# Optimization experiments

Hardware: AMD Instinct MI355X
Metric: run time of the kernel (lower is better)

The kernel has to match this reference:

```python
import jax, jax.numpy as jnp
import numpy as np

NUM_EXPERTS = 8
TOP_K = 2
HIDDEN = 1024
INTER = 2048
SHARED_INTER = 1024
T = 8192
STD = 0.02


def setup_inputs() -> dict:
    key = jax.random.key(0)
    ks = jax.random.split(key, 6)
    return {
        "hidden_states": jax.random.normal(ks[0], (T, HIDDEN), dtype=jnp.float32),
        "w_gate": jax.random.normal(ks[1], (NUM_EXPERTS, HIDDEN), dtype=jnp.float32) * STD,
        "w_fc": jax.random.normal(ks[2], (NUM_EXPERTS, INTER, HIDDEN), dtype=jnp.float32) * STD,
        "w_proj": jax.random.normal(ks[3], (NUM_EXPERTS, HIDDEN, INTER), dtype=jnp.float32) * (STD / np.sqrt(2 * 24)),
        "w_fc_shared": jax.random.normal(ks[4], (SHARED_INTER, HIDDEN), dtype=jnp.float32) * STD,
        "w_proj_shared": jax.random.normal(ks[5], (HIDDEN, SHARED_INTER), dtype=jnp.float32) * (STD / np.sqrt(2 * 24)),
    }


def reference(hidden_states, w_gate, w_fc, w_proj, w_fc_shared, w_proj_shared):
    x = hidden_states.reshape(-1, HIDDEN)  # [T, d]
    # --- routing: top-k over router logits, softmax over the k selected logits (fp32) ---
    router_logits = x @ w_gate.T  # [T, E]
    top_vals, top_idx = jax.lax.top_k(router_logits, TOP_K)  # [T, K]
    gates = jax.nn.softmax(top_vals.astype(jnp.float32), axis=-1).astype(x.dtype)  # [T, K]
    # --- expert FFN: dense per-expert compute, masked combine (== scatter/grouped-GEMM math) ---
    out = jnp.zeros_like(x)
    for e in range(NUM_EXPERTS):
        gate_e = jnp.sum(jnp.where(top_idx == e, gates, jnp.zeros_like(gates)), axis=-1)  # [T]
        h = jax.nn.gelu(x @ w_fc[e].T, approximate=False) @ w_proj[e].T  # [T, d]
        out = out + gate_e[:, None] * h
    # --- shared expert ---
    shared = jax.nn.gelu(x @ w_fc_shared.T, approximate=False) @ w_proj_shared.T
    return out + shared
```

## Files before the change

kernel.cpp:

```cpp
#include <hip/hip_runtime.h>
#include <cstdint>
#include <cstdio>

#define DEVI __device__ __forceinline__

constexpr int TOKS = 8192;
constexpr int HID  = 1024;
constexpr int INTR = 2048;
constexpr int SINT = 1024;
constexpr int NEXP = 8;
constexpr int MAXSLOT = 17408;

typedef __bf16 bf16x8 __attribute__((ext_vector_type(8)));
typedef float  f32x4  __attribute__((ext_vector_type(4)));

DEVI unsigned short f2bf(float f) {
  unsigned int u = __float_as_uint(f);
  u += 0x7FFFu + ((u >> 16) & 1u);
  return (unsigned short)(u >> 16);
}

DEVI float bf2f(unsigned short h) {
  return __uint_as_float((unsigned int)h << 16);
}

DEVI void gl_lds16(const unsigned short* g, unsigned short* l) {
  __attribute__((address_space(1))) uint32_t* gp =
      (__attribute__((address_space(1))) uint32_t*)(uintptr_t)g;
  __attribute__((address_space(3))) uint32_t* lp =
      (__attribute__((address_space(3))) uint32_t*)(uint32_t)(uintptr_t)l;
  __builtin_amdgcn_global_load_lds(gp, lp, 16, 0, 0);
}

DEVI float gelu_fast(float x) {
  const float z = fabsf(x) * 0.70710678118654752f;
  const float t = __builtin_amdgcn_rcpf(1.0f + 0.3275911f * z);
  float p = 1.061405429f;
  p = p * t - 1.453152027f;
  p = p * t + 1.421413741f;
  p = p * t - 0.284496736f;
  p = p * t + 0.254829592f;
  const float e = __builtin_amdgcn_exp2f(-z * z * 1.4426950408889634f);
  float erfz = 1.0f - p * t * e;
  erfz = copysignf(erfz, x);
  return 0.5f * x * (1.0f + erfz);
}

DEVI int xcd_chunk_map(int bid, int total) {
  const int q = total >> 3, r = total & 7;
  const int x = bid & 7, i = bid >> 3;
  return (x < r ? x * (q + 1) : r * (q + 1) + (x - r) * q) + i;
}

__global__ void k_f2bf_all(const float* __restrict__ s0, unsigned short* __restrict__ d0, int n0,
                           const float* __restrict__ s1, unsigned short* __restrict__ d1, int n1,
                           const float* __restrict__ s2, unsigned short* __restrict__ d2, int n2,
                           const float* __restrict__ s3, unsigned short* __restrict__ d3, int n3) {
  const int ntot = n0 + n1 + n2 + n3;
  int i = blockIdx.x * blockDim.x + threadIdx.x;
  const int stride = gridDim.x * blockDim.x;
  for (; i < ntot; i += stride) {
    int j = i;
    const float* s; unsigned short* d;
    if (j < n0) { s = s0; d = d0; }
    else if ((j -= n0) < n1) { s = s1; d = d1; }
    else if ((j -= n1) < n2) { s = s2; d = d2; }
    else { j -= n2; s = s3; d = d3; }
    float4 v = ((const float4*)s)[j];
    ushort4 o;
    o.x = f2bf(v.x); o.y = f2bf(v.y); o.z = f2bf(v.z); o.w = f2bf(v.w);
    ((ushort4*)d)[j] = o;
  }
}

__global__ __launch_bounds__(256) void k_router(
    const float* __restrict__ x, const float* __restrict__ wg,
    unsigned short* __restrict__ xb,
    int* __restrict__ rec_e, float2* __restrict__ rec_g) {
  const int wave = threadIdx.x >> 6;
  const int lane = threadIdx.x & 63;
  const int t = blockIdx.x * 4 + wave;

  float4 xv[4];
  const float4* x4 = (const float4*)(x + (size_t)t * HID);
#pragma unroll
  for (int j = 0; j < 4; ++j) xv[j] = x4[j * 64 + lane];

  ushort4* xb4 = (ushort4*)(xb + (size_t)t * HID);
#pragma unroll
  for (int j = 0; j < 4; ++j) {
    float4 v = xv[j];
    ushort4 o; o.x = f2bf(v.x); o.y = f2bf(v.y); o.z = f2bf(v.z); o.w = f2bf(v.w);
    xb4[j * 64 + lane] = o;
  }

  float lg[NEXP];
#pragma unroll
  for (int e = 0; e < NEXP; ++e) {
    const float4* w4 = (const float4*)(wg + (size_t)e * HID);
    float s = 0.f;
#pragma unroll
    for (int j = 0; j < 4; ++j) {
      float4 a = xv[j], b = w4[j * 64 + lane];
      s += a.x * b.x + a.y * b.y + a.z * b.z + a.w * b.w;
    }
    lg[e] = s;
  }
#pragma unroll
  for (int e = 0; e < NEXP; ++e)
#pragma unroll
    for (int off = 32; off > 0; off >>= 1) lg[e] += __shfl_xor(lg[e], off);

  if (lane == 0) {
    int b0 = 0; float v0 = lg[0];
    for (int e = 1; e < NEXP; ++e) if (lg[e] > v0) { v0 = lg[e]; b0 = e; }
    int b1 = -1; float v1 = -1e30f;
    for (int e = 0; e < NEXP; ++e) if (e != b0 && lg[e] > v1) { v1 = lg[e]; b1 = e; }
    const float d = expf(v1 - v0);
    const float g0 = 1.f / (1.f + d);
    const float g1 = d / (1.f + d);
    rec_e[t] = b0 | (b1 << 16);
    rec_g[t] = make_float2(g0, g1);
  }
}

__global__ __launch_bounds__(256) void k_count(
    const int* __restrict__ rec_e, int* __restrict__ rec_p, int* __restrict__ cnt) {
  __shared__ int hist[NEXP];
  __shared__ int base[NEXP];
  const int t = blockIdx.x * 256 + threadIdx.x;
  if (threadIdx.x < NEXP) hist[threadIdx.x] = 0;
  __syncthreads();
  const int ee = rec_e[t];
  const int e0 = ee & 0xffff, e1 = ee >> 16;
  const int r0 = atomicAdd(&hist[e0], 1);
  const int r1 = atomicAdd(&hist[e1], 1);
  __syncthreads();
  if (threadIdx.x < NEXP)
    base[threadIdx.x] = atomicAdd(&cnt[threadIdx.x], hist[threadIdx.x]);
  __syncthreads();
  rec_p[t] = (base[e0] + r0) | ((base[e1] + r1) << 16);
}

__global__ void k_scan(const int* __restrict__ cnt, int* __restrict__ offs) {
  if (threadIdx.x == 0 && blockIdx.x == 0) {
    int* tb0 = offs + 16;
    int* tb1 = offs + 32;
    int o = 0, t0 = 0, t1 = 0;
    tb0[0] = 0; tb1[0] = 0;
    for (int e = 0; e < NEXP; ++e) {
      offs[e] = o;
      const int mt = (cnt[e] + 127) >> 7;
      o += mt << 7;
      t0 += mt * (INTR / 128);
      t1 += mt * (HID / 128);
      tb0[e + 1] = t0;
      tb1[e + 1] = t1;
    }
    offs[NEXP] = o;
  }
}

__global__ void k_assign(const int* __restrict__ rec_e, const int* __restrict__ rec_p,
                         const int* __restrict__ offs, int* __restrict__ tok) {
  const int t = blockIdx.x * 256 + threadIdx.x;
  if (t >= TOKS) return;
  const int ee = rec_e[t], pp = rec_p[t];
  const int s0 = offs[ee & 0xffff] + (pp & 0xffff);
  const int s1 = offs[ee >> 16] + (pp >> 16);
  tok[s0] = t;
  tok[s1] = t;
}

template <int PHASE>
__global__ __launch_bounds__(256, 2) void k_gemmF(
    const unsigned short* __restrict__ Ae,
    const unsigned short* __restrict__ Be,
    unsigned short* __restrict__ He,
    const unsigned short* __restrict__ Ash,
    const unsigned short* __restrict__ Bsh,
    unsigned short* __restrict__ Hsh,
    const int* __restrict__ cnt,
    const int* __restrict__ offs,
    const int* __restrict__ tok) {
  constexpr int SH_TILES = (TOKS / 128) * 8;

  const int* tb = offs + ((PHASE == 0) ? 16 : 32);
  const int expTotal = tb[8];
  const int total = expTotal + SH_TILES;
  int bid = blockIdx.x;
  if (bid >= total) return;
  bid = xcd_chunk_map(bid, total);

  const unsigned short *A, *B;
  unsigned short* Hout;
  int count, gOff = 0, m0, n0, K, N;
  bool gather = false;
  if (bid < expTotal) {
    constexpr int NT_SHIFT = (PHASE == 0) ? 4 : 3;
    int e = 0;
    while (bid >= tb[e + 1]) ++e;
    const int local = bid - tb[e];
    count = cnt[e];
    const int off = offs[e];
    m0 = (local >> NT_SHIFT) << 7;
    n0 = (local & ((1 << NT_SHIFT) - 1)) << 7;
    K = (PHASE == 0) ? HID : INTR;
    N = (PHASE == 0) ? INTR : HID;
    if (PHASE == 0) { A = Ae; gather = true; gOff = off; }
    else            { A = Ae + (size_t)off * K; }
    B = Be + (size_t)e * (size_t)N * K;
    Hout = He + (size_t)off * N;
  } else {
    const int local = bid - expTotal;
    count = TOKS;
    m0 = (local >> 3) << 7;
    n0 = (local & 7) << 7;
    K = (PHASE == 0) ? HID : SINT;
    N = (PHASE == 0) ? SINT : HID;
    A = Ash; B = Bsh; Hout = Hsh;
  }

  __shared__ alignas(16) unsigned short As[2][128 * 64];
  __shared__ alignas(16) unsigned short Bs[2][128 * 64];

  const int tid = threadIdx.x;

  const int srow = tid >> 3;
  const int schunk = tid & 7;
  const unsigned short* gA[4];
  const unsigned short* gB[4];
#pragma unroll
  for (int r = 0; r < 4; ++r) {
    const int gr = r * 32 + srow;
    int mr = m0 + gr; if (mr > count - 1) mr = count - 1;
    const int row = gather ? tok[gOff + mr] : mr;
    const int sc = ((schunk ^ (gr & 7)) & 7) * 8;
    gA[r] = A + (size_t)row * (size_t)K + sc;
    gB[r] = B + (size_t)(n0 + gr) * (size_t)K + sc;
  }

  const int wid = tid >> 6;
  const int lane = tid & 63;
  const int wr = wid >> 1;
  const int wc = wid & 1;
  const int fm = lane & 15;
  const int fq = lane >> 4;
  int aOff[4], bOff[4];
#pragma unroll
  for (int i = 0; i < 4; ++i) {
    const int row = wr * 64 + i * 16 + fm;
    aOff[i] = row * 128 + ((fq ^ (row & 7)) * 16);
  }
#pragma unroll
  for (int j = 0; j < 4; ++j) {
    const int row = wc * 64 + j * 16 + fm;
    bOff[j] = row * 128 + ((fq ^ (row & 7)) * 16);
  }

  auto stage = [&](int buf, int k0) {
#pragma unroll
    for (int r = 0; r < 4; ++r)
      gl_lds16(gA[r] + k0, &As[buf][r * 2048 + tid * 8]);
#pragma unroll
    for (int r = 0; r < 4; ++r)
      gl_lds16(gB[r] + k0, &Bs[buf][r * 2048 + tid * 8]);
  };

  f32x4 acc[4][4] = {};

  stage(0, 0);
  __syncthreads();

  int cur = 0;
  for (int k0 = 0; k0 < K; k0 += 64) {
    const bool more = (k0 + 64 < K);
    if (more) stage(cur ^ 1, k0 + 64);

    const char* aBase = (const char*)&As[cur][0];
    const char* bBase = (const char*)&Bs[cur][0];
    __builtin_amdgcn_s_setprio(1);
#pragma unroll
    for (int s = 0; s < 2; ++s) {
      bf16x8 af[4], bfr[4];
#pragma unroll
      for (int i = 0; i < 4; ++i)
        af[i] = *(const bf16x8*)(aBase + (aOff[i] ^ (s << 6)));
#pragma unroll
      for (int j = 0; j < 4; ++j)
        bfr[j] = *(const bf16x8*)(bBase + (bOff[j] ^ (s << 6)));
#pragma unroll
      for (int i = 0; i < 4; ++i)
#pragma unroll
        for (int j = 0; j < 4; ++j)
          acc[i][j] = __builtin_amdgcn_mfma_f32_16x16x32_bf16(af[i], bfr[j], acc[i][j], 0, 0, 0);
    }
    __builtin_amdgcn_s_setprio(0);

    if (more) { __syncthreads(); cur ^= 1; }
  }

  constexpr bool GELU = (PHASE == 0);
#pragma unroll
  for (int i = 0; i < 4; ++i) {
#pragma unroll
    for (int rr = 0; rr < 4; ++rr) {
      const int m = m0 + wr * 64 + i * 16 + fq * 4 + rr;
      if (m < count) {
        unsigned short* orow = Hout + (size_t)m * N + (n0 + wc * 64 + fm);
#pragma unroll
        for (int j = 0; j < 4; ++j) {
          const float v = acc[i][j][rr];
          orow[j * 16] = f2bf(GELU ? gelu_fast(v) : v);
        }
      }
    }
  }
}

__global__ __launch_bounds__(256) void k_combine(
    const unsigned short* __restrict__ Y,
    const unsigned short* __restrict__ Ys,
    const int* __restrict__ rec_e, const int* __restrict__ rec_p,
    const float2* __restrict__ rec_g, const int* __restrict__ offs,
    float* __restrict__ out) {
  const int t = blockIdx.x;
  const int ee = rec_e[t], pp = rec_p[t];
  const float2 g = rec_g[t];
  const int s0 = offs[ee & 0xffff] + (pp & 0xffff);
  const int s1 = offs[ee >> 16] + (pp >> 16);
  const int c = threadIdx.x * 4;
  ushort4 a = *(const ushort4*)&Y[(size_t)s0 * HID + c];
  ushort4 b = *(const ushort4*)&Y[(size_t)s1 * HID + c];
  ushort4 s = *(const ushort4*)&Ys[(size_t)t * HID + c];
  float4 o;
  o.x = g.x * bf2f(a.x) + g.y * bf2f(b.x) + bf2f(s.x);
  o.y = g.x * bf2f(a.y) + g.y * bf2f(b.y) + bf2f(s.y);
  o.z = g.x * bf2f(a.z) + g.y * bf2f(b.z) + bf2f(s.z);
  o.w = g.x * bf2f(a.w) + g.y * bf2f(b.w) + bf2f(s.w);
  *(float4*)&out[(size_t)t * HID + c] = o;
}

extern "C" void kernel_launch(void* const* d_in, const int* in_sizes, int n_in,
                              void* d_out, int out_size, void* d_ws, size_t ws_size,
                              hipStream_t stream) {
  const float* x   = (const float*)d_in[0];
  const float* wg  = (const float*)d_in[1];
  const float* wfc = (const float*)d_in[2];
  const float* wpj = (const float*)d_in[3];
  const float* wfs = (const float*)d_in[4];
  const float* wps = (const float*)d_in[5];
  float* out = (float*)d_out;
  char* ws = (char*)d_ws;

  constexpr size_t OFF_XB   = 0;
  constexpr size_t OFF_WFC  = OFF_XB   + (size_t)TOKS * HID * 2;
  constexpr size_t OFF_WPJ  = OFF_WFC  + (size_t)NEXP * INTR * HID * 2;
  constexpr size_t OFF_WFS  = OFF_WPJ  + (size_t)NEXP * HID * INTR * 2;
  constexpr size_t OFF_WPS  = OFF_WFS  + (size_t)SINT * HID * 2;
  constexpr size_t OFF_H    = OFF_WPS  + (size_t)HID * SINT * 2;
  constexpr size_t OFF_HS   = OFF_H    + (size_t)MAXSLOT * INTR * 2;
  constexpr size_t OFF_Y    = OFF_HS   + (size_t)TOKS * SINT * 2;
  constexpr size_t OFF_YS   = OFF_Y    + (size_t)MAXSLOT * HID * 2;
  constexpr size_t OFF_CNT  = OFF_YS   + (size_t)TOKS * HID * 2;
  constexpr size_t OFF_OFFS = OFF_CNT  + 32;
  constexpr size_t OFF_RECE = OFF_OFFS + 256;
  constexpr size_t OFF_RECP = OFF_RECE + (size_t)TOKS * 4;
  constexpr size_t OFF_RECG = OFF_RECP + (size_t)TOKS * 4;
  constexpr size_t OFF_TOK  = OFF_RECG + (size_t)TOKS * 8;

  unsigned short* xb   = (unsigned short*)(ws + OFF_XB);
  unsigned short* wfcb = (unsigned short*)(ws + OFF_WFC);
  unsigned short* wpjb = (unsigned short*)(ws + OFF_WPJ);
  unsigned short* wfsb = (unsigned short*)(ws + OFF_WFS);
  unsigned short* wpsb = (unsigned short*)(ws + OFF_WPS);
  unsigned short* h    = (unsigned short*)(ws + OFF_H);
  unsigned short* hs   = (unsigned short*)(ws + OFF_HS);
  unsigned short* Y    = (unsigned short*)(ws + OFF_Y);
  unsigned short* Ys   = (unsigned short*)(ws + OFF_YS);
  int*    cnt   = (int*)(ws + OFF_CNT);
  int*    offs  = (int*)(ws + OFF_OFFS);
  int*    rec_e = (int*)(ws + OFF_RECE);
  int*    rec_p = (int*)(ws + OFF_RECP);
  float2* rec_g = (float2*)(ws + OFF_RECG);
  int*    tok   = (int*)(ws + OFF_TOK);

  hipMemsetAsync(cnt, 0, NEXP * sizeof(int), stream);

  k_f2bf_all<<<2048, 256, 0, stream>>>(
      wfc, wfcb, NEXP * INTR * HID / 4,
      wpj, wpjb, NEXP * HID * INTR / 4,
      wfs, wfsb, SINT * HID / 4,
      wps, wpsb, HID * SINT / 4);

  k_router<<<TOKS / 4, 256, 0, stream>>>(x, wg, xb, rec_e, rec_g);
  k_count<<<TOKS / 256, 256, 0, stream>>>(rec_e, rec_p, cnt);
  k_scan<<<1, 64, 0, stream>>>(cnt, offs);
  k_assign<<<TOKS / 256, 256, 0, stream>>>(rec_e, rec_p, offs, tok);

  constexpr int GRID_FC = 136 * (INTR / 128) + (TOKS / 128) * 8;
  constexpr int GRID_PJ = 136 * (HID  / 128) + (TOKS / 128) * 8;

  k_gemmF<0><<<GRID_FC, 256, 0, stream>>>(xb, wfcb, h, xb, wfsb, hs, cnt, offs, tok);
  k_gemmF<1><<<GRID_PJ, 256, 0, stream>>>(h, wpjb, Y, hs, wpsb, Ys, cnt, offs, tok);

  k_combine<<<TOKS, 256, 0, stream>>>(Y, Ys, rec_e, rec_p, rec_g, offs, out);
}
```

Before: 432.0 us.

## Fuse router with weight conversion and merge count/scan/assign into one sort kernel

Weight fp32-to-bf16 conversion is folded into the router kernel as extra blocks, so both run in one launch. The separate count, scan and assign kernels and the memset are replaced by a single 1024-thread block that builds per-expert histograms in shared memory, computes offsets, and writes absolute slot indices and the token map. Combine now reads precomputed absolute slots and no longer looks up offsets. This removes several launches and global round trips, but the sort phase now runs on a single block.

```diff
diff --git a/kernel.cpp b/kernel.cpp
--- a/kernel.cpp
+++ b/kernel.cpp
@@ -52,105 +52,111 @@
   return (x < r ? x * (q + 1) : r * (q + 1) + (x - r) * q) + i;
 }
 
-__global__ void k_f2bf_all(const float* __restrict__ s0, unsigned short* __restrict__ d0, int n0,
-                           const float* __restrict__ s1, unsigned short* __restrict__ d1, int n1,
-                           const float* __restrict__ s2, unsigned short* __restrict__ d2, int n2,
-                           const float* __restrict__ s3, unsigned short* __restrict__ d3, int n3) {
-  const int ntot = n0 + n1 + n2 + n3;
-  int i = blockIdx.x * blockDim.x + threadIdx.x;
-  const int stride = gridDim.x * blockDim.x;
-  for (; i < ntot; i += stride) {
-    int j = i;
-    const float* s; unsigned short* d;
-    if (j < n0) { s = s0; d = d0; }
-    else if ((j -= n0) < n1) { s = s1; d = d1; }
-    else if ((j -= n1) < n2) { s = s2; d = d2; }
-    else { j -= n2; s = s3; d = d3; }
-    float4 v = ((const float4*)s)[j];
-    ushort4 o;
-    o.x = f2bf(v.x); o.y = f2bf(v.y); o.z = f2bf(v.z); o.w = f2bf(v.w);
-    ((ushort4*)d)[j] = o;
-  }
-}
-
-__global__ __launch_bounds__(256) void k_router(
+__global__ __launch_bounds__(256) void k_fr(
     const float* __restrict__ x, const float* __restrict__ wg,
     unsigned short* __restrict__ xb,
-    int* __restrict__ rec_e, float2* __restrict__ rec_g) {
-  const int wave = threadIdx.x >> 6;
-  const int lane = threadIdx.x & 63;
-  const int t = blockIdx.x * 4 + wave;
-
-  float4 xv[4];
-  const float4* x4 = (const float4*)(x + (size_t)t * HID);
-#pragma unroll
-  for (int j = 0; j < 4; ++j) xv[j] = x4[j * 64 + lane];
-
-  ushort4* xb4 = (ushort4*)(xb + (size_t)t * HID);
-#pragma unroll
-  for (int j = 0; j < 4; ++j) {
-    float4 v = xv[j];
-    ushort4 o; o.x = f2bf(v.x); o.y = f2bf(v.y); o.z = f2bf(v.z); o.w = f2bf(v.w);
-    xb4[j * 64 + lane] = o;
-  }
-
-  float lg[NEXP];
-#pragma unroll
-  for (int e = 0; e < NEXP; ++e) {
-    const float4* w4 = (const float4*)(wg + (size_t)e * HID);
-    float s = 0.f;
+    int* __restrict__ rec_e, float2* __restrict__ rec_g,
+    const float* __restrict__ s0, unsigned short* __restrict__ d0, int n0,
+    const float* __restrict__ s1, unsigned short* __restrict__ d1, int n1,
+    const float* __restrict__ s2, unsigned short* __restrict__ d2, int n2,
+    const float* __restrict__ s3, unsigned short* __restrict__ d3, int n3) {
+  if (blockIdx.x < TOKS / 4) {
+    const int wave = threadIdx.x >> 6;
+    const int lane = threadIdx.x & 63;
+    const int t = blockIdx.x * 4 + wave;
+
+    float4 xv[4];
+    const float4* x4 = (const float4*)(x + (size_t)t * HID);
+#pragma unroll
+    for (int j = 0; j < 4; ++j) xv[j] = x4[j * 64 + lane];
+
+    ushort4* xb4 = (ushort4*)(xb + (size_t)t * HID);
 #pragma unroll
     for (int j = 0; j < 4; ++j) {
-      float4 a = xv[j], b = w4[j * 64 + lane];
-      s += a.x * b.x + a.y * b.y + a.z * b.z + a.w * b.w;
-    }
-    lg[e] = s;
-  }
-#pragma unroll
-  for (int e = 0; e < NEXP; ++e)
-#pragma unroll
-    for (int off = 32; off > 0; off >>= 1) lg[e] += __shfl_xor(lg[e], off);
-
-  if (lane == 0) {
-    int b0 = 0; float v0 = lg[0];
-    for (int e = 1; e < NEXP; ++e) if (lg[e] > v0) { v0 = lg[e]; b0 = e; }
-    int b1 = -1; float v1 = -1e30f;
-    for (int e = 0; e < NEXP; ++e) if (e != b0 && lg[e] > v1) { v1 = lg[e]; b1 = e; }
-    const float d = expf(v1 - v0);
-    const float g0 = 1.f / (1.f + d);
-    const float g1 = d / (1.f + d);
-    rec_e[t] = b0 | (b1 << 16);
-    rec_g[t] = make_float2(g0, g1);
-  }
-}
-
-__global__ __launch_bounds__(256) void k_count(
-    const int* __restrict__ rec_e, int* __restrict__ rec_p, int* __restrict__ cnt) {
-  __shared__ int hist[NEXP];
-  __shared__ int base[NEXP];
-  const int t = blockIdx.x * 256 + threadIdx.x;
-  if (threadIdx.x < NEXP) hist[threadIdx.x] = 0;
+      float4 v = xv[j];
+      ushort4 o; o.x = f2bf(v.x); o.y = f2bf(v.y); o.z = f2bf(v.z); o.w = f2bf(v.w);
+      xb4[j * 64 + lane] = o;
+    }
+
+    float lg[NEXP];
+#pragma unroll
+    for (int e = 0; e < NEXP; ++e) {
+      const float4* w4 = (const float4*)(wg + (size_t)e * HID);
+      float s = 0.f;
+#pragma unroll
+      for (int j = 0; j < 4; ++j) {
+        float4 a = xv[j], b = w4[j * 64 + lane];
+        s += a.x * b.x + a.y * b.y + a.z * b.z + a.w * b.w;
+      }
+      lg[e] = s;
+    }
+#pragma unroll
+    for (int e = 0; e < NEXP; ++e)
+#pragma unroll
+      for (int off = 32; off > 0; off >>= 1) lg[e] += __shfl_xor(lg[e], off);
+
+    if (lane == 0) {
+      int b0 = 0; float v0 = lg[0];
+      for (int e = 1; e < NEXP; ++e) if (lg[e] > v0) { v0 = lg[e]; b0 = e; }
+      int b1 = -1; float v1 = -1e30f;
+      for (int e = 0; e < NEXP; ++e) if (e != b0 && lg[e] > v1) { v1 = lg[e]; b1 = e; }
+      const float d = expf(v1 - v0);
+      const float g0 = 1.f / (1.f + d);
+      const float g1 = d / (1.f + d);
+      rec_e[t] = b0 | (b1 << 16);
+      rec_g[t] = make_float2(g0, g1);
+    }
+  } else {
+    const int nb = gridDim.x - TOKS / 4;
+    const int ntot = n0 + n1 + n2 + n3;
+    int i = (blockIdx.x - TOKS / 4) * 256 + threadIdx.x;
+    const int stride = nb * 256;
+    for (; i < ntot; i += stride) {
+      int j = i;
+      const float* s; unsigned short* d;
+      if (j < n0) { s = s0; d = d0; }
+      else if ((j -= n0) < n1) { s = s1; d = d1; }
+      else if ((j -= n1) < n2) { s = s2; d = d2; }
+      else { j -= n2; s = s3; d = d3; }
+      float4 v = ((const float4*)s)[j];
+      ushort4 o;
+      o.x = f2bf(v.x); o.y = f2bf(v.y); o.z = f2bf(v.z); o.w = f2bf(v.w);
+      ((ushort4*)d)[j] = o;
+    }
+  }
+}
+
+__global__ __launch_bounds__(1024) void k_sort(
+    const int* __restrict__ rec_e, int* __restrict__ rec_s,
+    int* __restrict__ cnt, int* __restrict__ offs, int* __restrict__ tok) {
+  __shared__ int hist[4][NEXP];
+  __shared__ int base[4][NEXP];
+  const int tid = threadIdx.x;
+  const int sub = tid & 3;
+  if (tid < 32) ((int*)hist)[tid] = 0;
   __syncthreads();
-  const int ee = rec_e[t];
-  const int e0 = ee & 0xffff, e1 = ee >> 16;
-  const int r0 = atomicAdd(&hist[e0], 1);
-  const int r1 = atomicAdd(&hist[e1], 1);
+  int e0[8], e1[8], r0[8], r1[8];
+#pragma unroll
+  for (int i = 0; i < 8; ++i) {
+    const int t = i * 1024 + tid;
+    const int ee = rec_e[t];
+    e0[i] = ee & 0xffff; e1[i] = ee >> 16;
+    r0[i] = atomicAdd(&hist[sub][e0[i]], 1);
+    r1[i] = atomicAdd(&hist[sub][e1[i]], 1);
+  }
   __syncthreads();
-  if (threadIdx.x < NEXP)
-    base[threadIdx.x] = atomicAdd(&cnt[threadIdx.x], hist[threadIdx.x]);
-  __syncthreads();
-  rec_p[t] = (base[e0] + r0) | ((base[e1] + r1) << 16);
-}
-
-__global__ void k_scan(const int* __restrict__ cnt, int* __restrict__ offs) {
-  if (threadIdx.x == 0 && blockIdx.x == 0) {
+  if (tid == 0) {
     int* tb0 = offs + 16;
     int* tb1 = offs + 32;
     int o = 0, t0 = 0, t1 = 0;
     tb0[0] = 0; tb1[0] = 0;
     for (int e = 0; e < NEXP; ++e) {
+      int c = 0;
+#pragma unroll
+      for (int j = 0; j < 4; ++j) { base[j][e] = o + c; c += hist[j][e]; }
+      cnt[e] = c;
       offs[e] = o;
-      const int mt = (cnt[e] + 127) >> 7;
+      const int mt = (c + 127) >> 7;
       o += mt << 7;
       t0 += mt * (INTR / 128);
       t1 += mt * (HID / 128);
@@ -159,17 +165,16 @@
     }
     offs[NEXP] = o;
   }
-}
-
-__global__ void k_assign(const int* __restrict__ rec_e, const int* __restrict__ rec_p,
-                         const int* __restrict__ offs, int* __restrict__ tok) {
-  const int t = blockIdx.x * 256 + threadIdx.x;
-  if (t >= TOKS) return;
-  const int ee = rec_e[t], pp = rec_p[t];
-  const int s0 = offs[ee & 0xffff] + (pp & 0xffff);
-  const int s1 = offs[ee >> 16] + (pp >> 16);
-  tok[s0] = t;
-  tok[s1] = t;
+  __syncthreads();
+#pragma unroll
+  for (int i = 0; i < 8; ++i) {
+    const int t = i * 1024 + tid;
+    const int S0 = base[sub][e0[i]] + r0[i];
+    const int S1 = base[sub][e1[i]] + r1[i];
+    rec_s[t] = S0 | (S1 << 16);
+    tok[S0] = t;
+    tok[S1] = t;
+  }
 }
 
 template <int PHASE>
@@ -321,14 +326,13 @@
 __global__ __launch_bounds__(256) void k_combine(
     const unsigned short* __restrict__ Y,
     const unsigned short* __restrict__ Ys,
-    const int* __restrict__ rec_e, const int* __restrict__ rec_p,
-    const float2* __restrict__ rec_g, const int* __restrict__ offs,
+    const int* __restrict__ rec_s, const float2* __restrict__ rec_g,
     float* __restrict__ out) {
   const int t = blockIdx.x;
-  const int ee = rec_e[t], pp = rec_p[t];
+  const int rs = rec_s[t];
   const float2 g = rec_g[t];
-  const int s0 = offs[ee & 0xffff] + (pp & 0xffff);
-  const int s1 = offs[ee >> 16] + (pp >> 16);
+  const int s0 = rs & 0xffff;
+  const int s1 = (rs >> 16) & 0xffff;
   const int c = threadIdx.x * 4;
   ushort4 a = *(const ushort4*)&Y[(size_t)s0 * HID + c];
   ushort4 b = *(const ushort4*)&Y[(size_t)s1 * HID + c];
@@ -365,8 +369,8 @@
   constexpr size_t OFF_CNT  = OFF_YS   + (size_t)TOKS * HID * 2;
   constexpr size_t OFF_OFFS = OFF_CNT  + 32;
   constexpr size_t OFF_RECE = OFF_OFFS + 256;
-  constexpr size_t OFF_RECP = OFF_RECE + (size_t)TOKS * 4;
-  constexpr size_t OFF_RECG = OFF_RECP + (size_t)TOKS * 4;
+  constexpr size_t OFF_RECS = OFF_RECE + (size_t)TOKS * 4;
+  constexpr size_t OFF_RECG = OFF_RECS + (size_t)TOKS * 4;
   constexpr size_t OFF_TOK  = OFF_RECG + (size_t)TOKS * 8;
 
   unsigned short* xb   = (unsigned short*)(ws + OFF_XB);
@@ -381,22 +385,18 @@
   int*    cnt   = (int*)(ws + OFF_CNT);
   int*    offs  = (int*)(ws + OFF_OFFS);
   int*    rec_e = (int*)(ws + OFF_RECE);
-  int*    rec_p = (int*)(ws + OFF_RECP);
+  int*    rec_s = (int*)(ws + OFF_RECS);
   float2* rec_g = (float2*)(ws + OFF_RECG);
   int*    tok   = (int*)(ws + OFF_TOK);
 
-  hipMemsetAsync(cnt, 0, NEXP * sizeof(int), stream);
-
-  k_f2bf_all<<<2048, 256, 0, stream>>>(
+  k_fr<<<TOKS / 4 + 2048, 256, 0, stream>>>(
+      x, wg, xb, rec_e, rec_g,
       wfc, wfcb, NEXP * INTR * HID / 4,
       wpj, wpjb, NEXP * HID * INTR / 4,
       wfs, wfsb, SINT * HID / 4,
       wps, wpsb, HID * SINT / 4);
 
-  k_router<<<TOKS / 4, 256, 0, stream>>>(x, wg, xb, rec_e, rec_g);
-  k_count<<<TOKS / 256, 256, 0, stream>>>(rec_e, rec_p, cnt);
-  k_scan<<<1, 64, 0, stream>>>(cnt, offs);
-  k_assign<<<TOKS / 256, 256, 0, stream>>>(rec_e, rec_p, offs, tok);
+  k_sort<<<1, 1024, 0, stream>>>(rec_e, rec_s, cnt, offs, tok);
 
   constexpr int GRID_FC = 136 * (INTR / 128) + (TOKS / 128) * 8;
   constexpr int GRID_PJ = 136 * (HID  / 128) + (TOKS / 128) * 8;
@@ -404,5 +404,5 @@
   k_gemmF<0><<<GRID_FC, 256, 0, stream>>>(xb, wfcb, h, xb, wfsb, hs, cnt, offs, tok);
   k_gemmF<1><<<GRID_PJ, 256, 0, stream>>>(h, wpjb, Y, hs, wpsb, Ys, cnt, offs, tok);
 
-  k_combine<<<TOKS, 256, 0, stream>>>(Y, Ys, rec_e, rec_p, rec_g, offs, out);
-}
+  k_combine<<<TOKS, 256, 0, stream>>>(Y, Ys, rec_s, rec_g, out);
+}
```

New measurement: 446.8 us. 1.03x slower.
